# Kernel tuning notes

Measured on AMD Instinct MI355X. Metric: run time of the kernel, lower is better.

Reference implementation:

```python
import jax, jax.numpy as jnp
import numpy as np

B, IN, H = 64, 1024, 1024

def _lin(x, W, b):
    # torch nn.Linear: y = x @ W.T + b, W:[out,in]
    return x @ W.T + b

def setup_inputs() -> dict:
    key = jax.random.key(0)
    ks = jax.random.split(key, 16)
    s_in = 1.0 / np.sqrt(IN)
    s_cat = 1.0 / np.sqrt(IN + H)
    s_h = 1.0 / np.sqrt(H)
    return {
        "x": jax.random.normal(ks[0], (B, IN), jnp.float32),
        "h": jax.random.normal(ks[1], (B, H), jnp.float32),
        "C": jax.random.normal(ks[2], (B, H, H), jnp.float32) * 0.02,
        "Wq": jax.random.normal(ks[3], (H, IN), jnp.float32) * s_in,
        "bq": jax.random.normal(ks[4], (H,), jnp.float32) * s_in,
        "Wk": jax.random.normal(ks[5], (H, IN), jnp.float32) * s_in,
        "bk": jax.random.normal(ks[6], (H,), jnp.float32) * s_in,
        "Wv": jax.random.normal(ks[7], (H, IN), jnp.float32) * s_in,
        "bv": jax.random.normal(ks[8], (H,), jnp.float32) * s_in,
        "Wf": jax.random.normal(ks[9], (H, IN + H), jnp.float32) * s_cat,
        "bf": jax.random.normal(ks[10], (H,), jnp.float32) * s_cat,
        "Wi": jax.random.normal(ks[11], (H, IN + H), jnp.float32) * s_cat,
        "bi": jax.random.normal(ks[12], (H,), jnp.float32) * s_cat,
        "Wo": jax.random.normal(ks[13], (H, H), jnp.float32) * s_h,
        "bo": jax.random.normal(ks[14], (H,), jnp.float32) * s_h,
    }

def reference(x, h, C, Wq, bq, Wk, bk, Wv, bv, Wf, bf, Wi, bi, Wo, bo):
    q = _lin(x, Wq, bq)            # [B,H]
    k = _lin(x, Wk, bk)            # [B,H]
    v = _lin(x, Wv, bv)            # [B,H]
    combined = jnp.concatenate([x, h], axis=-1)       # [B,IN+H]
    f = jax.nn.sigmoid(_lin(combined, Wf, bf))        # [B,H]
    i = jax.nn.sigmoid(_lin(combined, Wi, bi))        # [B,H]
    # gated matrix-memory update: C_new[b,m,n] = f[b,m]*C[b,m,n] + i[b,m]*k[b,m]*v[b,n]
    C_new = f[:, :, None] * C + (i * k)[:, :, None] * v[:, None, :]
    # readout: matvec with q then tanh and output projection
    r = jnp.einsum('bmn,bn->bm', C_new, q)            # [B,H]
    h_new = _lin(jnp.tanh(r), Wo, bo)                 # [B,H]
    return (h_new, C_new)
```

## Files before the change

kernel.cpp:

```cpp
#include <hip/hip_runtime.h>
#include <math.h>

#define HB 64
#define HD 1024
#define KS 128
#define XS 68

typedef float f32x4 __attribute__((ext_vector_type(4)));

__device__ __forceinline__ void splitk_tile(
    const float* __restrict__ X0, int noff,
    const float* __restrict__ W, int K,
    int m0, int k0,
    float* __restrict__ P)
{
    __shared__ __align__(16) float Xs[32][XS];
    __shared__ __align__(16) float Ws[32][XS];
    const int t  = threadIdx.x;
    const int bx = t >> 4;
    const int my = t & 15;
    float acc[4][4] = {};

    float4 xp[2], wp[2];
    #pragma unroll
    for (int i = 0; i < 2; ++i) {
        int u = t + 256 * i;
        int r = u >> 3, nq = u & 7;
        xp[i] = *(const float4*)&X0[r * HD + (k0 - noff) + nq * 4];
        wp[i] = *(const float4*)&W[(long long)(m0 + r) * K + k0 + nq * 4];
    }

    for (int kc = 0; kc < KS; kc += 32) {
        #pragma unroll
        for (int i = 0; i < 2; ++i) {
            int u = t + 256 * i;
            int r = u >> 3, nq = u & 7;
            Xs[nq * 4 + 0][r] = xp[i].x; Xs[nq * 4 + 1][r] = xp[i].y;
            Xs[nq * 4 + 2][r] = xp[i].z; Xs[nq * 4 + 3][r] = xp[i].w;
            Ws[nq * 4 + 0][r] = wp[i].x; Ws[nq * 4 + 1][r] = wp[i].y;
            Ws[nq * 4 + 2][r] = wp[i].z; Ws[nq * 4 + 3][r] = wp[i].w;
        }
        __syncthreads();
        if (kc + 32 < KS) {
            const int n0 = k0 + kc + 32;
            #pragma unroll
            for (int i = 0; i < 2; ++i) {
                int u = t + 256 * i;
                int r = u >> 3, nq = u & 7;
                xp[i] = *(const float4*)&X0[r * HD + (n0 - noff) + nq * 4];
                wp[i] = *(const float4*)&W[(long long)(m0 + r) * K + n0 + nq * 4];
            }
        }
        #pragma unroll
        for (int n = 0; n < 32; ++n) {
            float4 xv = *(const float4*)&Xs[n][bx * 4];
            float4 wv = *(const float4*)&Ws[n][my * 4];
            float xe[4] = {xv.x, xv.y, xv.z, xv.w};
            float we[4] = {wv.x, wv.y, wv.z, wv.w};
            #pragma unroll
            for (int i = 0; i < 4; ++i)
                #pragma unroll
                for (int j = 0; j < 4; ++j)
                    acc[i][j] = fmaf(xe[i], we[j], acc[i][j]);
        }
        __syncthreads();
    }
    #pragma unroll
    for (int i = 0; i < 4; ++i) {
        float4 o4 = make_float4(acc[i][0], acc[i][1], acc[i][2], acc[i][3]);
        *(float4*)&P[(bx * 4 + i) * HD + m0 + my * 4] = o4;
    }
}

__global__ __launch_bounds__(256) void qkvfi_splitk(
    const float* __restrict__ x, const float* __restrict__ h,
    const float* __restrict__ Wq, const float* __restrict__ Wk,
    const float* __restrict__ Wv, const float* __restrict__ Wf,
    const float* __restrict__ Wi, float* __restrict__ P)
{
    const int gy = blockIdx.y;
    const float* W; int K, split;
    if (gy < 24) {
        int g = gy >> 3; split = gy & 7; K = HD;
        W = (g == 0) ? Wq : (g == 1) ? Wk : Wv;
    } else {
        int tt = gy - 24; int g = tt >> 4; split = tt & 15; K = 2 * HD;
        W = g ? Wi : Wf;
    }
    const int k0 = split * KS;
    const float* X0; int noff;
    if (k0 < HD) { X0 = x; noff = 0; } else { X0 = h; noff = HD; }
    splitk_tile(X0, noff, W, K, blockIdx.x * 64, k0, P + (size_t)gy * (HB * HD));
}

__global__ __launch_bounds__(256) void out_splitk(
    const float* __restrict__ tr, const float* __restrict__ Wo,
    float* __restrict__ P2)
{
    const int split = blockIdx.y;
    splitk_tile(tr, 0, Wo, HD, blockIdx.x * 64, split * KS,
                P2 + (size_t)split * (HB * HD));
}

__global__ __launch_bounds__(256) void reduce_qkvfi(
    const float* __restrict__ P,
    const float* __restrict__ bq, const float* __restrict__ bk,
    const float* __restrict__ bv, const float* __restrict__ bfv,
    const float* __restrict__ biv,
    float* __restrict__ q, float* __restrict__ k, float* __restrict__ v,
    float* __restrict__ fg, float* __restrict__ ig)
{
    const int o4 = blockIdx.x * 256 + threadIdx.x;
    const int g  = o4 >> 14;
    const int r4 = o4 & 16383;
    const int m4 = r4 & 255;
    int base, ns, act; const float* bias; float* out;
    switch (g) {
        case 0:  base = 0;  ns = 8;  bias = bq;  out = q;  act = 0; break;
        case 1:  base = 8;  ns = 8;  bias = bk;  out = k;  act = 0; break;
        case 2:  base = 16; ns = 8;  bias = bv;  out = v;  act = 0; break;
        case 3:  base = 24; ns = 16; bias = bfv; out = fg; act = 1; break;
        default: base = 40; ns = 16; bias = biv; out = ig; act = 1; break;
    }
    float4 s = ((const float4*)bias)[m4];
    const float4* P4 = (const float4*)P;
    for (int i = 0; i < ns; ++i) {
        float4 p = P4[(size_t)(base + i) * 16384 + r4];
        s.x += p.x; s.y += p.y; s.z += p.z; s.w += p.w;
    }
    if (act) {
        s.x = 1.0f / (1.0f + expf(-s.x)); s.y = 1.0f / (1.0f + expf(-s.y));
        s.z = 1.0f / (1.0f + expf(-s.z)); s.w = 1.0f / (1.0f + expf(-s.w));
    }
    ((float4*)out)[r4] = s;
}

__global__ __launch_bounds__(256) void reduce_out(
    const float* __restrict__ P2, const float* __restrict__ bo,
    float* __restrict__ hnew)
{
    const int o4 = blockIdx.x * 256 + threadIdx.x;
    const int m4 = o4 & 255;
    float4 s = ((const float4*)bo)[m4];
    const float4* P4 = (const float4*)P2;
    #pragma unroll
    for (int i = 0; i < 8; ++i) {
        float4 p = P4[(size_t)i * 16384 + o4];
        s.x += p.x; s.y += p.y; s.z += p.z; s.w += p.w;
    }
    ((float4*)hnew)[o4] = s;
}

__global__ __launch_bounds__(256) void update_kernel(
    const float* __restrict__ C,
    const float* __restrict__ q, const float* __restrict__ k,
    const float* __restrict__ v, const float* __restrict__ fg,
    const float* __restrict__ ig,
    float* __restrict__ Cn, float* __restrict__ tr)
{
    __shared__ __align__(16) float qs[HD];
    __shared__ __align__(16) float vs[HD];
    const int t    = threadIdx.x;
    const int lane = t & 63;
    const int wid  = t >> 6;
    const int blk  = blockIdx.x;
    const int b    = blk >> 6;
    const int mt   = blk & 63;

    ((float4*)qs)[t] = ((const float4*)q)[b * 256 + t];
    ((float4*)vs)[t] = ((const float4*)v)[b * 256 + t];

    const int r0 = b * HD + mt * 16 + wid * 4;
    float f_[4], ik_[4];
    #pragma unroll
    for (int rr = 0; rr < 4; ++rr) {
        f_[rr]  = fg[r0 + rr];
        ik_[rr] = ig[r0 + rr] * k[r0 + rr];
    }
    __syncthreads();

    const f32x4* C4 = (const f32x4*)C;
    f32x4*       N4 = (f32x4*)Cn;
    const f32x4* q4s = (const f32x4*)qs;
    const f32x4* v4s = (const f32x4*)vs;

    float racc[4] = {0.f, 0.f, 0.f, 0.f};
    #pragma unroll
    for (int j = 0; j < 4; ++j) {
        const int o = lane + 64 * j;
        f32x4 cc[4];
        #pragma unroll
        for (int rr = 0; rr < 4; ++rr)
            cc[rr] = __builtin_nontemporal_load(&C4[(r0 + rr) * 256 + o]);
        f32x4 v4 = v4s[o];
        f32x4 q4 = q4s[o];
        #pragma unroll
        for (int rr = 0; rr < 4; ++rr) {
            f32x4 nn;
            nn.x = fmaf(f_[rr], cc[rr].x, ik_[rr] * v4.x);
            nn.y = fmaf(f_[rr], cc[rr].y, ik_[rr] * v4.y);
            nn.z = fmaf(f_[rr], cc[rr].z, ik_[rr] * v4.z);
            nn.w = fmaf(f_[rr], cc[rr].w, ik_[rr] * v4.w);
            __builtin_nontemporal_store(nn, &N4[(r0 + rr) * 256 + o]);
            racc[rr] += nn.x * q4.x + nn.y * q4.y + nn.z * q4.z + nn.w * q4.w;
        }
    }
    #pragma unroll
    for (int off = 32; off; off >>= 1) {
        #pragma unroll
        for (int rr = 0; rr < 4; ++rr)
            racc[rr] += __shfl_xor(racc[rr], off);
    }
    if (lane == 0) {
        #pragma unroll
        for (int rr = 0; rr < 4; ++rr)
            tr[r0 + rr] = tanhf(racc[rr]);
    }
}

extern "C" void kernel_launch(void* const* d_in, const int* in_sizes, int n_in,
                              void* d_out, int out_size, void* d_ws, size_t ws_size,
                              hipStream_t stream) {
    const float* x  = (const float*)d_in[0];
    const float* h  = (const float*)d_in[1];
    const float* C  = (const float*)d_in[2];
    const float* Wq = (const float*)d_in[3];
    const float* bq = (const float*)d_in[4];
    const float* Wk = (const float*)d_in[5];
    const float* bk = (const float*)d_in[6];
    const float* Wv = (const float*)d_in[7];
    const float* bv = (const float*)d_in[8];
    const float* Wf = (const float*)d_in[9];
    const float* bf = (const float*)d_in[10];
    const float* Wi = (const float*)d_in[11];
    const float* bi = (const float*)d_in[12];
    const float* Wo = (const float*)d_in[13];
    const float* bo = (const float*)d_in[14];

    float* outp = (float*)d_out;
    float* hnew = outp;
    float* Cn   = outp + HB * HD;

    const size_t SL = (size_t)HB * HD;
    float* ws = (float*)d_ws;
    float* q  = ws + 0 * SL;
    float* k  = ws + 1 * SL;
    float* v  = ws + 2 * SL;
    float* fg = ws + 3 * SL;
    float* ig = ws + 4 * SL;
    float* tr = ws + 5 * SL;
    float* P  = ws + 6 * SL;
    float* P2 = ws + 62 * SL;

    qkvfi_splitk<<<dim3(16, 56), 256, 0, stream>>>(x, h, Wq, Wk, Wv, Wf, Wi, P);
    reduce_qkvfi<<<dim3(320), 256, 0, stream>>>(P, bq, bk, bv, bf, bi,
                                                q, k, v, fg, ig);
    update_kernel<<<dim3((HB * HD) / 16), 256, 0, stream>>>(
        C, q, k, v, fg, ig, Cn, tr);
    out_splitk<<<dim3(16, 8), 256, 0, stream>>>(tr, Wo, P2);
    reduce_out<<<dim3(64), 256, 0, stream>>>(P2, bo, hnew);
}
```

Before: 145.7 us.

## Halve split-K count for projections, swap thread mapping, one row per wave in update

Split-K depth for the q/k/v/f/i projections doubles, so half as many blocks run and half as many partial slices are written and summed in the reduction. The thread-to-tile mapping in the shared GEMM tile is swapped between the batch and output axes. The update kernel now handles one C row per wavefront instead of four, launching four times more blocks. Fewer partials cut memory traffic, at the cost of fewer projection blocks to fill the GPU and more small blocks in the update pass, each reloading q and v into LDS.

```diff
diff --git a/kernel.cpp b/kernel.cpp
--- a/kernel.cpp
+++ b/kernel.cpp
@@ -3,11 +3,13 @@
 
 #define HB 64
 #define HD 1024
-#define KS 128
+#define KSF 256
+#define KSB 128
 #define XS 68
 
 typedef float f32x4 __attribute__((ext_vector_type(4)));
 
+template<int KS>
 __device__ __forceinline__ void splitk_tile(
     const float* __restrict__ X0, int noff,
     const float* __restrict__ W, int K,
@@ -17,8 +19,8 @@
     __shared__ __align__(16) float Xs[32][XS];
     __shared__ __align__(16) float Ws[32][XS];
     const int t  = threadIdx.x;
-    const int bx = t >> 4;
-    const int my = t & 15;
+    const int bx = t & 15;
+    const int my = t >> 4;
     float acc[4][4] = {};
 
     float4 xp[2], wp[2];
@@ -80,17 +82,18 @@
 {
     const int gy = blockIdx.y;
     const float* W; int K, split;
-    if (gy < 24) {
-        int g = gy >> 3; split = gy & 7; K = HD;
+    if (gy < 12) {
+        int g = gy >> 2; split = gy & 3; K = HD;
         W = (g == 0) ? Wq : (g == 1) ? Wk : Wv;
     } else {
-        int tt = gy - 24; int g = tt >> 4; split = tt & 15; K = 2 * HD;
+        int tt = gy - 12; int g = tt >> 3; split = tt & 7; K = 2 * HD;
         W = g ? Wi : Wf;
     }
-    const int k0 = split * KS;
+    const int k0 = split * KSF;
     const float* X0; int noff;
     if (k0 < HD) { X0 = x; noff = 0; } else { X0 = h; noff = HD; }
-    splitk_tile(X0, noff, W, K, blockIdx.x * 64, k0, P + (size_t)gy * (HB * HD));
+    splitk_tile<KSF>(X0, noff, W, K, blockIdx.x * 64, k0,
+                     P + (size_t)gy * (HB * HD));
 }
 
 __global__ __launch_bounds__(256) void out_splitk(
@@ -98,8 +101,8 @@
     float* __restrict__ P2)
 {
     const int split = blockIdx.y;
-    splitk_tile(tr, 0, Wo, HD, blockIdx.x * 64, split * KS,
-                P2 + (size_t)split * (HB * HD));
+    splitk_tile<KSB>(tr, 0, Wo, HD, blockIdx.x * 64, split * KSB,
+                     P2 + (size_t)split * (HB * HD));
 }
 
 __global__ __launch_bounds__(256) void reduce_qkvfi(
@@ -116,11 +119,11 @@
     const int m4 = r4 & 255;
     int base, ns, act; const float* bias; float* out;
     switch (g) {
-        case 0:  base = 0;  ns = 8;  bias = bq;  out = q;  act = 0; break;
-        case 1:  base = 8;  ns = 8;  bias = bk;  out = k;  act = 0; break;
-        case 2:  base = 16; ns = 8;  bias = bv;  out = v;  act = 0; break;
-        case 3:  base = 24; ns = 16; bias = bfv; out = fg; act = 1; break;
-        default: base = 40; ns = 16; bias = biv; out = ig; act = 1; break;
+        case 0:  base = 0;  ns = 4; bias = bq;  out = q;  act = 0; break;
+        case 1:  base = 4;  ns = 4; bias = bk;  out = k;  act = 0; break;
+        case 2:  base = 8;  ns = 4; bias = bv;  out = v;  act = 0; break;
+        case 3:  base = 12; ns = 8; bias = bfv; out = fg; act = 1; break;
+        default: base = 20; ns = 8; bias = biv; out = ig; act = 1; break;
     }
     float4 s = ((const float4*)bias)[m4];
     const float4* P4 = (const float4*)P;
@@ -161,61 +164,44 @@
     __shared__ __align__(16) float qs[HD];
     __shared__ __align__(16) float vs[HD];
     const int t    = threadIdx.x;
+    const int wid  = t >> 6;
     const int lane = t & 63;
-    const int wid  = t >> 6;
-    const int blk  = blockIdx.x;
-    const int b    = blk >> 6;
-    const int mt   = blk & 63;
+    const int row  = blockIdx.x * 4 + wid;
+    const int b    = row >> 10;
+    const int m    = row & (HD - 1);
 
     ((float4*)qs)[t] = ((const float4*)q)[b * 256 + t];
     ((float4*)vs)[t] = ((const float4*)v)[b * 256 + t];
 
-    const int r0 = b * HD + mt * 16 + wid * 4;
-    float f_[4], ik_[4];
-    #pragma unroll
-    for (int rr = 0; rr < 4; ++rr) {
-        f_[rr]  = fg[r0 + rr];
-        ik_[rr] = ig[r0 + rr] * k[r0 + rr];
-    }
+    const float fm  = fg[b * HD + m];
+    const float ikm = ig[b * HD + m] * k[b * HD + m];
     __syncthreads();
 
     const f32x4* C4 = (const f32x4*)C;
+    const f32x4* V4 = (const f32x4*)vs;
+    const f32x4* Q4 = (const f32x4*)qs;
     f32x4*       N4 = (f32x4*)Cn;
-    const f32x4* q4s = (const f32x4*)qs;
-    const f32x4* v4s = (const f32x4*)vs;
-
-    float racc[4] = {0.f, 0.f, 0.f, 0.f};
+
+    const int base = row * (HD / 4);
+
+    float racc = 0.f;
     #pragma unroll
     for (int j = 0; j < 4; ++j) {
-        const int o = lane + 64 * j;
-        f32x4 cc[4];
-        #pragma unroll
-        for (int rr = 0; rr < 4; ++rr)
-            cc[rr] = __builtin_nontemporal_load(&C4[(r0 + rr) * 256 + o]);
-        f32x4 v4 = v4s[o];
-        f32x4 q4 = q4s[o];
-        #pragma unroll
-        for (int rr = 0; rr < 4; ++rr) {
-            f32x4 nn;
-            nn.x = fmaf(f_[rr], cc[rr].x, ik_[rr] * v4.x);
-            nn.y = fmaf(f_[rr], cc[rr].y, ik_[rr] * v4.y);
-            nn.z = fmaf(f_[rr], cc[rr].z, ik_[rr] * v4.z);
-            nn.w = fmaf(f_[rr], cc[rr].w, ik_[rr] * v4.w);
-            __builtin_nontemporal_store(nn, &N4[(r0 + rr) * 256 + o]);
-            racc[rr] += nn.x * q4.x + nn.y * q4.y + nn.z * q4.z + nn.w * q4.w;
-        }
-    }
-    #pragma unroll
-    for (int off = 32; off; off >>= 1) {
-        #pragma unroll
-        for (int rr = 0; rr < 4; ++rr)
-            racc[rr] += __shfl_xor(racc[rr], off);
-    }
-    if (lane == 0) {
-        #pragma unroll
-        for (int rr = 0; rr < 4; ++rr)
-            tr[r0 + rr] = tanhf(racc[rr]);
-    }
+        int o = lane + 64 * j;
+        f32x4 c4 = __builtin_nontemporal_load(&C4[base + o]);
+        f32x4 v4 = V4[o];
+        f32x4 q4 = Q4[o];
+        f32x4 cn;
+        cn.x = fmaf(fm, c4.x, ikm * v4.x);
+        cn.y = fmaf(fm, c4.y, ikm * v4.y);
+        cn.z = fmaf(fm, c4.z, ikm * v4.z);
+        cn.w = fmaf(fm, c4.w, ikm * v4.w);
+        __builtin_nontemporal_store(cn, &N4[base + o]);
+        racc += cn.x * q4.x + cn.y * q4.y + cn.z * q4.z + cn.w * q4.w;
+    }
+    #pragma unroll
+    for (int off = 32; off; off >>= 1) racc += __shfl_xor(racc, off);
+    if (lane == 0) tr[row] = tanhf(racc);
 }
 
 extern "C" void kernel_launch(void* const* d_in, const int* in_sizes, int n_in,
@@ -250,12 +236,12 @@
     float* ig = ws + 4 * SL;
     float* tr = ws + 5 * SL;
     float* P  = ws + 6 * SL;
-    float* P2 = ws + 62 * SL;
-
-    qkvfi_splitk<<<dim3(16, 56), 256, 0, stream>>>(x, h, Wq, Wk, Wv, Wf, Wi, P);
+    float* P2 = ws + 34 * SL;
+
+    qkvfi_splitk<<<dim3(16, 28), 256, 0, stream>>>(x, h, Wq, Wk, Wv, Wf, Wi, P);
     reduce_qkvfi<<<dim3(320), 256, 0, stream>>>(P, bq, bk, bv, bf, bi,
                                                 q, k, v, fg, ig);
-    update_kernel<<<dim3((HB * HD) / 16), 256, 0, stream>>>(
+    update_kernel<<<dim3((HB * HD) / 4), 256, 0, stream>>>(
         C, q, k, v, fg, ig, Cn, tr);
     out_splitk<<<dim3(16, 8), 256, 0, stream>>>(tr, Wo, P2);
     reduce_out<<<dim3(64), 256, 0, stream>>>(P2, bo, hnew);
```

New measurement: 125.0 us. 14.3% less time.
